# Optimization experiments

Measured on AMD Instinct MI355X. Metric: run time of the kernel, lower is better.

Reference implementation:

```python
import jax, jax.numpy as jnp
import numpy as np

REPEAT = 75  # upsample_repeat
UP = 4       # upsample_convs[0]


def setup_inputs() -> dict:
    key = jax.random.key(0)
    ks = jax.random.split(key, 12)
    B, L, F = 4, 48, 80
    C, H, A = 256, 896, 256  # conditional_size, rnn_size, signal_channels
    T = L * UP * REPEAT
    def xav(k, shape, fan_in):
        return jax.random.normal(k, shape, jnp.float32) * (1.0 / np.sqrt(fan_in))
    return {
        "local_features": jax.random.normal(ks[0], (B, L, F), jnp.float32),
        "gold_signal": jax.random.uniform(ks[1], (B, T), jnp.float32, -1.0, 1.0),
        "proj_w": xav(ks[2], (C, F), F),
        "proj_b": jnp.zeros((C,), jnp.float32),
        "up_w": xav(ks[3], (C, C, UP), C),
        "up_b": jnp.zeros((C,), jnp.float32),
        "embed_w": xav(ks[4], (C,), 1),
        "embed_b": jnp.zeros((C,), jnp.float32),
        "gru_wi": xav(ks[5], (3 * H, C), C),
        "gru_wh": xav(ks[6], (3 * H, H), H),
        "gru_bi": jnp.zeros((3 * H,), jnp.float32),
        "gru_bh": jnp.zeros((3 * H,), jnp.float32),
        "out_w1": xav(ks[7], (H, H), H),
        "out_b1": jnp.zeros((H,), jnp.float32),
        "out_w2": xav(ks[8], (A, H), H),
        "out_b2": jnp.zeros((A,), jnp.float32),
    }


def _forward(local_features, gold_signal, proj_w, proj_b, up_w, up_b,
             embed_w, embed_b, gru_wi, gru_wh, gru_bi, gru_bh,
             out_w1, out_b1, out_w2, out_b2):
    B = local_features.shape[0]
    O = up_w.shape[0]
    # --- conditional feature upsample ---
    # 1x1 conv: [B,L,F] -> [B,C,L]
    x = jnp.einsum("blf,cf->bcl", local_features, proj_w) + proj_b[None, :, None]
    # transposed conv, kernel=stride=UP: [B,C,L] -> [B,C,L*UP]
    x = jnp.einsum("bcl,ock->bolk", x, up_w).reshape(B, O, -1) + up_b[None, :, None]
    cond = jnp.repeat(x, REPEAT, axis=2)  # [B,C,T]
    # --- embed gold signal (1x1 conv, in_channels=1) ---
    sig = gold_signal[:, None, :] * embed_w[None, :, None] + embed_b[None, :, None]
    feats = (sig + cond).transpose(2, 0, 1)  # [T,B,C]
    # --- GRU (torch semantics), precompute input projections ---
    xp = feats @ gru_wi.T + gru_bi  # [T,B,3H]
    H = gru_wh.shape[1]

    def step(h, xpt):
        gh = h @ gru_wh.T + gru_bh
        xr, xz, xn = jnp.split(xpt, 3, axis=-1)
        hr, hz, hn = jnp.split(gh, 3, axis=-1)
        r = jax.nn.sigmoid(xr + hr)
        z = jax.nn.sigmoid(xz + hz)
        n = jnp.tanh(xn + r * hn)
        h_new = (1.0 - z) * n + z * h
        return h_new, h_new

    h0 = jnp.zeros((B, H), feats.dtype)
    _, hs = jax.lax.scan(step, h0, xp)  # [T,B,H]
    # --- output MLP + log-softmax over channels ---
    y = jax.nn.relu(hs @ out_w1.T + out_b1)
    logits = y @ out_w2.T + out_b2  # [T,B,A]
    logp = jax.nn.log_softmax(logits, axis=2)
    return logp.transpose(1, 2, 0)  # [B,A,T]


def reference(local_features, gold_signal, proj_w, proj_b, up_w, up_b,
              embed_w, embed_b, gru_wi, gru_wh, gru_bi, gru_bh,
              out_w1, out_b1, out_w2, out_b2):
    return _forward(local_features, gold_signal, proj_w, proj_b, up_w, up_b,
                    embed_w, embed_b, gru_wi, gru_wh, gru_bi, gru_bh,
                    out_w1, out_b1, out_w2, out_b2)
```

## Files before the change

### kernel.cpp

```cpp
#include <hip/hip_runtime.h>
#include <hip/hip_bf16.h>

#define B_ 4
#define L_ 48
#define F_ 80
#define C_ 256
#define H_ 896
#define G3_ 2688
#define A_ 256
#define T_ 14400
#define NBLK_ 192
#define REP_ 75

#define NMEM 28
#define RPW 12
#define NREAL 112
#define GRU_GRID 256
#define DYN_LDS 81920

typedef _Float16 __attribute__((ext_vector_type(8))) f16x8;
typedef __attribute__((ext_vector_type(4))) float f32x4;
typedef _Float16 __attribute__((ext_vector_type(2))) half2_;

__device__ __forceinline__ float fdot2f16(unsigned int a, unsigned int b, float c){
  return __builtin_amdgcn_fdot2(__builtin_bit_cast(half2_, a), __builtin_bit_cast(half2_, b), c, false);
}
__device__ __forceinline__ unsigned short f2h(float x){
  return __builtin_bit_cast(unsigned short, (_Float16)x);
}
__device__ __forceinline__ unsigned int packh2(float a, float b){
  return (unsigned int)f2h(a) | ((unsigned int)f2h(b) << 16);
}

template<int CTRL>
__device__ __forceinline__ float dppadd(float x){
  int r = __builtin_amdgcn_update_dpp(0, __builtin_bit_cast(int, x), CTRL, 0xF, 0xF, true);
  return x + __builtin_bit_cast(float, r);
}
__device__ __forceinline__ float wred(float x){
  x = dppadd<0xB1>(x);
  x = dppadd<0x4E>(x);
  x = dppadd<0x124>(x);
  x = dppadd<0x128>(x);
  x = dppadd<0x142>(x);
  x = dppadd<0x143>(x);
  return x;
}

__device__ __forceinline__ void ld7_llc(const unsigned int* base, unsigned int* hd){
  asm volatile(
    "global_load_dword %0, %7, off sc0 sc1\n\t"
    "global_load_dword %1, %7, off offset:256 sc0 sc1\n\t"
    "global_load_dword %2, %7, off offset:512 sc0 sc1\n\t"
    "global_load_dword %3, %7, off offset:768 sc0 sc1\n\t"
    "global_load_dword %4, %7, off offset:1024 sc0 sc1\n\t"
    "global_load_dword %5, %7, off offset:1280 sc0 sc1\n\t"
    "global_load_dword %6, %7, off offset:1536 sc0 sc1\n\t"
    "s_waitcnt vmcnt(0)"
    : "=&v"(hd[0]), "=&v"(hd[1]), "=&v"(hd[2]), "=&v"(hd[3]),
      "=&v"(hd[4]), "=&v"(hd[5]), "=&v"(hd[6])
    : "v"(base)
    : "memory");
}

__global__ void k_transpose_pw(const float* __restrict__ pw, float* __restrict__ pwT){
  int idx = blockIdx.x * 256 + threadIdx.x;
  if (idx >= F_ * C_) return;
  int f = idx / C_, c = idx % C_;
  pwT[idx] = pw[c * F_ + f];
}

__global__ void k_x1(const float* __restrict__ lf, const float* __restrict__ pwT,
                     const float* __restrict__ pb, float* __restrict__ x1){
  int bl = blockIdx.x;
  int c = threadIdx.x;
  const float* lrow = lf + (size_t)bl * F_;
  float acc = pb[c];
  for (int f = 0; f < F_; ++f) acc = fmaf(lrow[f], pwT[f * C_ + c], acc);
  x1[(size_t)bl * C_ + c] = acc;
}

__global__ void k_transpose_up(const float* __restrict__ up, float* __restrict__ upT){
  int idx = blockIdx.x * 256 + threadIdx.x;
  int o = idx % C_, c = (idx / C_) % C_, k = idx / (C_ * C_);
  upT[idx] = up[(o * C_ + c) * 4 + k];
}

__global__ void k_cond(const float* __restrict__ upT, const float* __restrict__ x1,
                       const float* __restrict__ ub, float* __restrict__ cond){
  int bblk = blockIdx.x;
  int blk = bblk % NBLK_;
  int b = bblk / NBLK_;
  int l = blk >> 2, kk = blk & 3;
  int o = threadIdx.x;
  const float* x1row = x1 + ((size_t)b * L_ + l) * C_;
  const float* uT = upT + (size_t)kk * C_ * C_;
  float acc = ub[o];
  for (int c = 0; c < C_; ++c) acc = fmaf(x1row[c], uT[c * C_ + o], acc);
  cond[(size_t)bblk * C_ + o] = acc;
}

__global__ void k_transpose_wi(const float* __restrict__ wi, float* __restrict__ wiT){
  int idx = blockIdx.x * 256 + threadIdx.x;
  int g = idx % G3_, c = idx / G3_;
  wiT[idx] = wi[(size_t)g * C_ + c];
}

__global__ void k_v(const float* __restrict__ wiT, const float* __restrict__ eb,
                    const float* __restrict__ cond, const float* __restrict__ bi,
                    float* __restrict__ v){
  int idx = blockIdx.x * 512 + threadIdx.x;
  int g = idx % G3_;
  int bblk = idx / G3_;
  const float* crow = cond + (size_t)bblk * C_;
  float acc = bi[g];
  for (int c = 0; c < C_; ++c) acc = fmaf(eb[c] + crow[c], wiT[(size_t)c * G3_ + g], acc);
  v[idx] = acc;
}

__global__ void k_u(const float* __restrict__ wiT, const float* __restrict__ ew,
                    float* __restrict__ u){
  int g = blockIdx.x * 256 + threadIdx.x;
  if (g >= G3_) return;
  float acc = 0.f;
  for (int c = 0; c < C_; ++c) acc = fmaf(ew[c], wiT[(size_t)c * G3_ + g], acc);
  u[g] = acc;
}

__global__ void k_packwh(const float* __restrict__ wh, unsigned int* __restrict__ whp){
  int idx = blockIdx.x * 256 + threadIdx.x;
  int lane = idx & 63;
  int r2 = idx >> 6;
  int dw = r2 % 7; int r3 = r2 / 7;
  int i = r3 % RPW; int W = r3 / RPW;
  int g = (i >> 2) * H_ + W * 4 + (i & 3);
  int k = dw * 128 + lane * 2;
  const float* p = wh + (size_t)g * H_ + k;
  whp[idx] = packh2(p[0], p[1]);
}

__global__ void k_cvth(const float* __restrict__ src, unsigned short* __restrict__ dst, int n){
  int idx = blockIdx.x * 256 + threadIdx.x;
  if (idx >= n) return;
  dst[idx] = f2h(src[idx]);
}

__global__ __launch_bounds__(576, 1) void k_gru(
    const float* __restrict__ gold, const float* __restrict__ v,
    const float* __restrict__ u, const float* __restrict__ bh,
    const unsigned int* __restrict__ whp,
    unsigned short* hsx)
{
  extern __shared__ unsigned int dynls[];
  const int bid = blockIdx.x;
  const int tid = threadIdx.x;
  const int wave = tid >> 6;
  const int lane = tid & 63;

  if (bid >= NREAL){
    volatile unsigned int* bflag = dynls;
    if (tid == 0) dynls[0] = 0;
    __syncthreads();
    const unsigned int* slotT = (const unsigned int*)(hsx + ((size_t)T_ * B_) * H_);
    float x = 1.0f + (float)tid * 1e-6f;
    float a = 1.0000001f, b = 0.9999999f;
    for (;;){
#pragma unroll 64
      for (int i = 0; i < 4096; ++i)
        asm volatile("v_fmac_f32 %0, %1, %2" : "+v"(x) : "v"(a), "v"(b));
      if (wave == 0){
        unsigned int d = ~0u;
        if (lane < 4){
          const unsigned int* pp = slotT + lane * 448;
          asm volatile("global_load_dword %0, %1, off sc0 sc1\n\ts_waitcnt vmcnt(0)"
                       : "=v"(d) : "v"(pp) : "memory");
        }
        bool ok = (lane < 4) ? (d != ~0u) : true;
        if (__all(ok) && lane == 0) *bflag = 1u;
      }
      if (*bflag) break;
    }
    return;
  }

  const int batch = (bid & 7) >> 1;
  const int m = ((bid >> 3) << 1) | (bid & 1);
  unsigned int (*lds_h)[448] = (unsigned int(*)[448])dynls;

  if (wave == 8){
    for (int t = 0; t < T_; ++t){
      const unsigned int* hp =
          (const unsigned int*)(hsx + ((size_t)t * B_ + batch) * H_) + lane;
      unsigned int hd[7];
      for (;;){
        ld7_llc(hp, hd);
        bool ok = (hd[0] != ~0u) & (hd[1] != ~0u) & (hd[2] != ~0u) &
                  (hd[3] != ~0u) & (hd[4] != ~0u) & (hd[5] != ~0u) & (hd[6] != ~0u);
        if (__all(ok)) break;
      }
#pragma unroll
      for (int dw = 0; dw < 7; ++dw) lds_h[t & 1][dw * 64 + lane] = hd[dw];
      __syncthreads();
    }
    return;
  }

  const int W = m * 8 + wave;

  unsigned int wreg[RPW][7];
#pragma unroll
  for (int i = 0; i < RPW; ++i){
    const unsigned int* p = whp + ((size_t)(W * RPW + i) * 7) * 64 + lane;
#pragma unroll
    for (int dw = 0; dw < 7; ++dw) wreg[i][dw] = p[dw * 64];
  }

  const bool owner = (lane >= 48) && (lane < 52);
  const int jj = lane - 48;
  const int jg = 4 * W + (jj & 3);
  float u3[3] = {0,0,0}, bh3[3] = {0,0,0}, v3[3] = {0,0,0}, v3n[3] = {0,0,0};
  float hcur = 0.f;
  if (owner){
    u3[0] = u[jg]; u3[1] = u[jg + H_]; u3[2] = u[jg + 2 * H_];
    bh3[0] = bh[jg]; bh3[1] = bh[jg + H_]; bh3[2] = bh[jg + 2 * H_];
    const float* vp = v + ((size_t)(batch * NBLK_)) * G3_ + jg;
    v3[0] = vp[0]; v3[1] = vp[H_]; v3[2] = vp[2 * H_];
  }
  const float* goldb = gold + (size_t)batch * T_;
  int cnt = 0, blkc = 0;

  for (int t = 0; t < T_; ++t){
    float go = goldb[t];
    __syncthreads();
    unsigned int hd[7];
#pragma unroll
    for (int dw = 0; dw < 7; ++dw) hd[dw] = lds_h[t & 1][dw * 64 + lane];

    float acc[RPW];
#pragma unroll
    for (int i = 0; i < RPW; ++i){
      float a = 0.f;
#pragma unroll
      for (int dw = 0; dw < 7; ++dw) a = fdot2f16(wreg[i][dw], hd[dw], a);
      acc[i] = wred(a);
    }

    if (owner){
      if (cnt == REP_ - 2){
        int nb = blkc + 1; if (nb > NBLK_ - 1) nb = NBLK_ - 1;
        const float* vp = v + ((size_t)(batch * NBLK_ + nb)) * G3_ + jg;
        v3n[0] = vp[0]; v3n[1] = vp[H_]; v3n[2] = vp[2 * H_];
      }
      float hr = jj==0 ? acc[0] : jj==1 ? acc[1] : jj==2 ? acc[2]  : acc[3];
      float hz = jj==0 ? acc[4] : jj==1 ? acc[5] : jj==2 ? acc[6]  : acc[7];
      float hn = jj==0 ? acc[8] : jj==1 ? acc[9] : jj==2 ? acc[10] : acc[11];
      hr += bh3[0]; hz += bh3[1]; hn += bh3[2];
      float xr = fmaf(go, u3[0], v3[0]);
      float xz = fmaf(go, u3[1], v3[1]);
      float xn = fmaf(go, u3[2], v3[2]);
      float r = 1.f / (1.f + __expf(-(xr + hr)));
      float z = 1.f / (1.f + __expf(-(xz + hz)));
      float e = __expf(2.f * (xn + r * hn));
      float n = 1.f - 2.f / (e + 1.f);
      float hnew = (1.f - z) * n + z * hcur;
      hcur = hnew;
      unsigned int h16 = (unsigned int)f2h(hnew);
      unsigned int oth = (unsigned int)__builtin_amdgcn_update_dpp(
          0, (int)h16, 0xB1, 0xF, 0xF, true);
      unsigned int packed = h16 | (oth << 16);
      unsigned int p23 = (unsigned int)__builtin_amdgcn_update_dpp(
          0, (int)packed, 0x4E, 0xF, 0xF, true);
      if (jj == 0){
        unsigned long long v64 = (unsigned long long)packed
                               | ((unsigned long long)p23 << 32);
        unsigned long long* dst =
            (unsigned long long*)((unsigned int*)(hsx + ((size_t)(t + 1) * B_ + batch) * H_)
                                  + 2 * W);
        __hip_atomic_store(dst, v64, __ATOMIC_RELAXED, __HIP_MEMORY_SCOPE_AGENT);
      }
    }
    if (++cnt == REP_){
      cnt = 0; ++blkc;
      v3[0] = v3n[0]; v3[1] = v3n[1]; v3[2] = v3n[2];
    }
  }
}

__global__ __launch_bounds__(256) void k_mlp(
    const unsigned short* hs, const unsigned short* __restrict__ w1h,
    const unsigned short* __restrict__ w2h, const float* __restrict__ ob1,
    const float* __restrict__ ob2, float* logits)
{
  const int mtile = blockIdx.x * 32;
  const int tid = threadIdx.x;
  const int wid = tid >> 6, lane = tid & 63;
  const int l15 = lane & 15, l4 = lane >> 4;
  __shared__ unsigned short y_lds[32 * 904];

  for (int nblk = 0; nblk < 14; ++nblk){
    f32x4 acc[2] = {(f32x4)(0.f), (f32x4)(0.f)};
    const int colg = nblk * 64 + wid * 16 + l15;
    for (int kk = 0; kk < 28; ++kk){
      const int k = kk * 32 + l4 * 8;
      f16x8 bfrag = *(const f16x8*)(w1h + (size_t)colg * H_ + k);
#pragma unroll
      for (int mf = 0; mf < 2; ++mf){
        f16x8 afrag = *(const f16x8*)(hs + (size_t)(mtile + mf * 16 + l15) * H_ + k);
        acc[mf] = __builtin_amdgcn_mfma_f32_16x16x32_f16(afrag, bfrag, acc[mf], 0, 0, 0);
      }
    }
    float bias = ob1[colg];
#pragma unroll
    for (int mf = 0; mf < 2; ++mf)
#pragma unroll
      for (int rg = 0; rg < 4; ++rg){
        float yv = acc[mf][rg] + bias;
        yv = yv > 0.f ? yv : 0.f;
        y_lds[(mf * 16 + l4 * 4 + rg) * 904 + colg] = f2h(yv);
      }
  }
  __syncthreads();

  f32x4 a2acc[2][4];
#pragma unroll
  for (int mf = 0; mf < 2; ++mf)
#pragma unroll
    for (int nf = 0; nf < 4; ++nf) a2acc[mf][nf] = (f32x4)(0.f);

  for (int kk = 0; kk < 28; ++kk){
    const int k = kk * 32 + l4 * 8;
    f16x8 a2[2];
#pragma unroll
    for (int mf = 0; mf < 2; ++mf)
      a2[mf] = *(const f16x8*)(&y_lds[(mf * 16 + l15) * 904 + k]);
#pragma unroll
    for (int nf = 0; nf < 4; ++nf){
      const int col = wid * 64 + nf * 16 + l15;
      f16x8 bfrag = *(const f16x8*)(w2h + (size_t)col * H_ + k);
#pragma unroll
      for (int mf = 0; mf < 2; ++mf)
        a2acc[mf][nf] = __builtin_amdgcn_mfma_f32_16x16x32_f16(a2[mf], bfrag, a2acc[mf][nf], 0, 0, 0);
    }
  }
#pragma unroll
  for (int nf = 0; nf < 4; ++nf){
    const int col = wid * 64 + nf * 16 + l15;
    const float bias = ob2[col];
#pragma unroll
    for (int mf = 0; mf < 2; ++mf)
#pragma unroll
      for (int rg = 0; rg < 4; ++rg){
        const int mrow = mtile + mf * 16 + l4 * 4 + rg;
        logits[(size_t)mrow * 448 + col] = a2acc[mf][nf][rg] + bias;
      }
  }
}

__global__ __launch_bounds__(256) void k_softmax(const float* __restrict__ logits,
                                                 float* __restrict__ out)
{
  const int bid = blockIdx.x;
  const int b = bid / 225;
  const int t0 = (bid % 225) * 64;
  const int tid = threadIdx.x;
  __shared__ float pm[64][4];
  __shared__ float ps[64][4];
  __shared__ float lz[64];
  {
    const int r = tid >> 2, q = tid & 3;
    const float* row = logits + (size_t)((t0 + r) * 4 + b) * 448 + q * 64;
    float mx = -1e30f;
    for (int j = 0; j < 64; ++j) mx = fmaxf(mx, row[j]);
    float s = 0.f;
    for (int j = 0; j < 64; ++j) s += __expf(row[j] - mx);
    pm[r][q] = mx; ps[r][q] = s;
  }
  __syncthreads();
  if (tid < 64){
    float m0 = pm[tid][0], m1 = pm[tid][1], m2 = pm[tid][2], m3 = pm[tid][3];
    float mx = fmaxf(fmaxf(m0, m1), fmaxf(m2, m3));
    float s = ps[tid][0] * __expf(m0 - mx) + ps[tid][1] * __expf(m1 - mx)
            + ps[tid][2] * __expf(m2 - mx) + ps[tid][3] * __expf(m3 - mx);
    lz[tid] = mx + logf(s);
  }
  __syncthreads();
  for (int i = 0; i < 64; ++i){
    const int idx = i * 256 + tid;
    const int a = idx >> 6, tt = idx & 63;
    float x = logits[(size_t)((t0 + tt) * 4 + b) * 448 + a];
    out[((size_t)(b * A_) + a) * T_ + t0 + tt] = x - lz[tt];
  }
}

extern "C" void kernel_launch(void* const* d_in, const int* in_sizes, int n_in,
                              void* d_out, int out_size, void* d_ws, size_t ws_size,
                              hipStream_t stream)
{
  (void)in_sizes; (void)n_in; (void)out_size; (void)ws_size;
  const float* lf   = (const float*)d_in[0];
  const float* gold = (const float*)d_in[1];
  const float* pw   = (const float*)d_in[2];
  const float* pb   = (const float*)d_in[3];
  const float* upw  = (const float*)d_in[4];
  const float* upb  = (const float*)d_in[5];
  const float* ew   = (const float*)d_in[6];
  const float* eb   = (const float*)d_in[7];
  const float* wi   = (const float*)d_in[8];
  const float* wh   = (const float*)d_in[9];
  const float* bi   = (const float*)d_in[10];
  const float* bhp  = (const float*)d_in[11];
  const float* w1   = (const float*)d_in[12];
  const float* b1   = (const float*)d_in[13];
  const float* w2   = (const float*)d_in[14];
  const float* b2   = (const float*)d_in[15];
  float* out = (float*)d_out;
  char* ws = (char*)d_ws;

  size_t off = 0;
  auto take = [&](size_t bytes){
    size_t r = off; off += (bytes + 255) & ~(size_t)255; return r;
  };
  float* pwT  = (float*)(ws + take((size_t)F_ * C_ * 4));
  float* x1   = (float*)(ws + take((size_t)B_ * L_ * C_ * 4));
  float* upT  = (float*)(ws + take((size_t)4 * C_ * C_ * 4));
  float* cond = (float*)(ws + take((size_t)B_ * NBLK_ * C_ * 4));
  float* wiT  = (float*)(ws + take((size_t)C_ * G3_ * 4));
  float* v    = (float*)(ws + take((size_t)B_ * NBLK_ * G3_ * 4));
  float* u    = (float*)(ws + take((size_t)G3_ * 4));
  unsigned int*   whp = (unsigned int*)(ws + take((size_t)224 * RPW * 7 * 64 * 4));
  unsigned short* w1h = (unsigned short*)(ws + take((size_t)H_ * H_ * 2));
  unsigned short* w2h = (unsigned short*)(ws + take((size_t)A_ * H_ * 2));
  unsigned short* hsx = (unsigned short*)(ws + take((size_t)(T_ + 1) * B_ * H_ * 2));

  hipFuncSetAttribute((const void*)k_gru,
                      hipFuncAttributeMaxDynamicSharedMemorySize, DYN_LDS);

  hipMemsetAsync((void*)hsx, 0, (size_t)B_ * H_ * 2, stream);
  hipMemsetAsync((void*)(hsx + (size_t)B_ * H_), 0xFF, (size_t)T_ * B_ * H_ * 2, stream);

  k_transpose_pw<<<80, 256, 0, stream>>>(pw, pwT);
  k_x1<<<B_ * L_, 256, 0, stream>>>(lf, pwT, pb, x1);
  k_transpose_up<<<1024, 256, 0, stream>>>(upw, upT);
  k_cond<<<B_ * NBLK_, 256, 0, stream>>>(upT, x1, upb, cond);
  k_transpose_wi<<<2688, 256, 0, stream>>>(wi, wiT);
  k_v<<<4032, 512, 0, stream>>>(wiT, eb, cond, bi, v);
  k_u<<<11, 256, 0, stream>>>(wiT, ew, u);
  k_packwh<<<4704, 256, 0, stream>>>(wh, whp);
  k_cvth<<<(H_ * H_ + 255) / 256, 256, 0, stream>>>(w1, w1h, H_ * H_);
  k_cvth<<<(A_ * H_ + 255) / 256, 256, 0, stream>>>(w2, w2h, A_ * H_);

  k_gru<<<GRU_GRID, 576, DYN_LDS, stream>>>(gold, v, u, bhp, whp, hsx);

  const unsigned short* hs_mlp = hsx + (size_t)B_ * H_;
  float* logits = (float*)hsx + (size_t)B_ * 448;
  k_mlp<<<1800, 256, 0, stream>>>(hs_mlp, w1h, w2h, b1, b2, logits);
  k_softmax<<<900, 256, 0, stream>>>(logits, out);
}
```

Baseline: 37.48 ms.

## Fuse output MLP into GRU kernel as concurrent consumer blocks

The spare blocks of the persistent GRU launch used to spin on dummy FMAs. They now run the output MLP tile by tile, each tile starting once the hidden states it needs have been published (polled with a sleep backoff). This overlaps the MLP with the serial recurrence and removes the separate MLP launch. The LDS-feeding wave also issues coherent prefetch loads a few steps ahead to warm the cache. The risks are that logits are written in place over hidden-state rows while the GRU is still running, and that the extra memory traffic and lost heater blocks may slow the latency-critical recurrence.

```diff
diff --git a/kernel.cpp b/kernel.cpp
--- a/kernel.cpp
+++ b/kernel.cpp
@@ -15,8 +15,8 @@
 #define NMEM 28
 #define RPW 12
 #define NREAL 112
-#define GRU_GRID 256
-#define DYN_LDS 81920
+#define NMLP 128
+#define NTILE 1800
 
 typedef _Float16 __attribute__((ext_vector_type(8))) f16x8;
 typedef __attribute__((ext_vector_type(4))) float f32x4;
@@ -148,44 +148,107 @@
 __global__ __launch_bounds__(576, 1) void k_gru(
     const float* __restrict__ gold, const float* __restrict__ v,
     const float* __restrict__ u, const float* __restrict__ bh,
-    const unsigned int* __restrict__ whp,
-    unsigned short* hsx)
+    const unsigned int* __restrict__ whp, unsigned short* hsx,
+    const unsigned short* __restrict__ w1h, const unsigned short* __restrict__ w2h,
+    const float* __restrict__ ob1, const float* __restrict__ ob2,
+    float* logits)
 {
-  extern __shared__ unsigned int dynls[];
+  __shared__ __attribute__((aligned(16))) unsigned char smem[32 * 904 * 2];
   const int bid = blockIdx.x;
   const int tid = threadIdx.x;
   const int wave = tid >> 6;
   const int lane = tid & 63;
 
   if (bid >= NREAL){
-    volatile unsigned int* bflag = dynls;
-    if (tid == 0) dynls[0] = 0;
-    __syncthreads();
-    const unsigned int* slotT = (const unsigned int*)(hsx + ((size_t)T_ * B_) * H_);
-    float x = 1.0f + (float)tid * 1e-6f;
-    float a = 1.0000001f, b = 0.9999999f;
-    for (;;){
-#pragma unroll 64
-      for (int i = 0; i < 4096; ++i)
-        asm volatile("v_fmac_f32 %0, %1, %2" : "+v"(x) : "v"(a), "v"(b));
+    unsigned short* y_lds = (unsigned short*)smem;
+    const unsigned short* hs = hsx + (size_t)B_ * H_;
+    const int wid = tid >> 6;
+    const int l15 = lane & 15, l4 = lane >> 4;
+    for (int k2 = bid - NREAL; k2 < NTILE; k2 += NMLP){
       if (wave == 0){
-        unsigned int d = ~0u;
-        if (lane < 4){
-          const unsigned int* pp = slotT + lane * 448;
-          asm volatile("global_load_dword %0, %1, off sc0 sc1\n\ts_waitcnt vmcnt(0)"
-                       : "=v"(d) : "v"(pp) : "memory");
+        const unsigned int* sp0 =
+            (const unsigned int*)(hsx + ((size_t)(8 * k2 + 8) * B_) * H_);
+        for (;;){
+          unsigned int hd[7]; bool ok = true;
+#pragma unroll
+          for (int b = 0; b < B_; ++b){
+            ld7_llc(sp0 + (size_t)b * 448 + lane, hd);
+            ok &= (hd[0]!=~0u)&(hd[1]!=~0u)&(hd[2]!=~0u)&(hd[3]!=~0u)
+                 &(hd[4]!=~0u)&(hd[5]!=~0u)&(hd[6]!=~0u);
+          }
+          if (__all(ok)) break;
+          __builtin_amdgcn_s_sleep(127);
         }
-        bool ok = (lane < 4) ? (d != ~0u) : true;
-        if (__all(ok) && lane == 0) *bflag = 1u;
-      }
-      if (*bflag) break;
+      }
+      __syncthreads();
+      const int mtile = k2 * 32;
+      if (tid < 256){
+        for (int nblk = 0; nblk < 14; ++nblk){
+          f32x4 acc[2] = {(f32x4)(0.f), (f32x4)(0.f)};
+          const int colg = nblk * 64 + wid * 16 + l15;
+          for (int kk = 0; kk < 28; ++kk){
+            const int k = kk * 32 + l4 * 8;
+            f16x8 bfrag = *(const f16x8*)(w1h + (size_t)colg * H_ + k);
+#pragma unroll
+            for (int mf = 0; mf < 2; ++mf){
+              f16x8 afrag = *(const f16x8*)(hs + (size_t)(mtile + mf * 16 + l15) * H_ + k);
+              acc[mf] = __builtin_amdgcn_mfma_f32_16x16x32_f16(afrag, bfrag, acc[mf], 0, 0, 0);
+            }
+          }
+          float bias = ob1[colg];
+#pragma unroll
+          for (int mf = 0; mf < 2; ++mf)
+#pragma unroll
+            for (int rg = 0; rg < 4; ++rg){
+              float yv = acc[mf][rg] + bias;
+              yv = yv > 0.f ? yv : 0.f;
+              y_lds[(mf * 16 + l4 * 4 + rg) * 904 + colg] = f2h(yv);
+            }
+        }
+      }
+      __syncthreads();
+      if (tid < 256){
+        f32x4 a2acc[2][4];
+#pragma unroll
+        for (int mf = 0; mf < 2; ++mf)
+#pragma unroll
+          for (int nf = 0; nf < 4; ++nf) a2acc[mf][nf] = (f32x4)(0.f);
+        for (int kk = 0; kk < 28; ++kk){
+          const int k = kk * 32 + l4 * 8;
+          f16x8 a2[2];
+#pragma unroll
+          for (int mf = 0; mf < 2; ++mf)
+            a2[mf] = *(const f16x8*)(&y_lds[(mf * 16 + l15) * 904 + k]);
+#pragma unroll
+          for (int nf = 0; nf < 4; ++nf){
+            const int col = wid * 64 + nf * 16 + l15;
+            f16x8 bfrag = *(const f16x8*)(w2h + (size_t)col * H_ + k);
+#pragma unroll
+            for (int mf = 0; mf < 2; ++mf)
+              a2acc[mf][nf] = __builtin_amdgcn_mfma_f32_16x16x32_f16(a2[mf], bfrag, a2acc[mf][nf], 0, 0, 0);
+          }
+        }
+#pragma unroll
+        for (int nf = 0; nf < 4; ++nf){
+          const int col = wid * 64 + nf * 16 + l15;
+          const float bias = ob2[col];
+#pragma unroll
+          for (int mf = 0; mf < 2; ++mf)
+#pragma unroll
+            for (int rg = 0; rg < 4; ++rg){
+              const int mrow = mtile + mf * 16 + l4 * 4 + rg;
+              logits[(size_t)mrow * 448 + col] = a2acc[mf][nf][rg] + bias;
+            }
+        }
+      }
+      __syncthreads();
     }
     return;
   }
 
   const int batch = (bid & 7) >> 1;
   const int m = ((bid >> 3) << 1) | (bid & 1);
-  unsigned int (*lds_h)[448] = (unsigned int(*)[448])dynls;
+  unsigned int (*lds_h)[448] = (unsigned int(*)[448])smem;
 
   if (wave == 8){
     for (int t = 0; t < T_; ++t){
@@ -200,6 +263,17 @@
       }
 #pragma unroll
       for (int dw = 0; dw < 7; ++dw) lds_h[t & 1][dw * 64 + lane] = hd[dw];
+      {
+        int tw = t + 4; if (tw > T_) tw = T_;
+        const unsigned int* wp =
+            (const unsigned int*)(hsx + ((size_t)tw * B_ + batch) * H_) + lane;
+#pragma unroll
+        for (int dw = 0; dw < 7; ++dw){
+          unsigned int dummy;
+          asm volatile("global_load_dword %0, %1, off sc0 sc1"
+                       : "=v"(dummy) : "v"(wp + dw * 64) : "memory");
+        }
+      }
       __syncthreads();
     }
     return;
@@ -286,76 +360,6 @@
   }
 }
 
-__global__ __launch_bounds__(256) void k_mlp(
-    const unsigned short* hs, const unsigned short* __restrict__ w1h,
-    const unsigned short* __restrict__ w2h, const float* __restrict__ ob1,
-    const float* __restrict__ ob2, float* logits)
-{
-  const int mtile = blockIdx.x * 32;
-  const int tid = threadIdx.x;
-  const int wid = tid >> 6, lane = tid & 63;
-  const int l15 = lane & 15, l4 = lane >> 4;
-  __shared__ unsigned short y_lds[32 * 904];
-
-  for (int nblk = 0; nblk < 14; ++nblk){
-    f32x4 acc[2] = {(f32x4)(0.f), (f32x4)(0.f)};
-    const int colg = nblk * 64 + wid * 16 + l15;
-    for (int kk = 0; kk < 28; ++kk){
-      const int k = kk * 32 + l4 * 8;
-      f16x8 bfrag = *(const f16x8*)(w1h + (size_t)colg * H_ + k);
-#pragma unroll
-      for (int mf = 0; mf < 2; ++mf){
-        f16x8 afrag = *(const f16x8*)(hs + (size_t)(mtile + mf * 16 + l15) * H_ + k);
-        acc[mf] = __builtin_amdgcn_mfma_f32_16x16x32_f16(afrag, bfrag, acc[mf], 0, 0, 0);
-      }
-    }
-    float bias = ob1[colg];
-#pragma unroll
-    for (int mf = 0; mf < 2; ++mf)
-#pragma unroll
-      for (int rg = 0; rg < 4; ++rg){
-        float yv = acc[mf][rg] + bias;
-        yv = yv > 0.f ? yv : 0.f;
-        y_lds[(mf * 16 + l4 * 4 + rg) * 904 + colg] = f2h(yv);
-      }
-  }
-  __syncthreads();
-
-  f32x4 a2acc[2][4];
-#pragma unroll
-  for (int mf = 0; mf < 2; ++mf)
-#pragma unroll
-    for (int nf = 0; nf < 4; ++nf) a2acc[mf][nf] = (f32x4)(0.f);
-
-  for (int kk = 0; kk < 28; ++kk){
-    const int k = kk * 32 + l4 * 8;
-    f16x8 a2[2];
-#pragma unroll
-    for (int mf = 0; mf < 2; ++mf)
-      a2[mf] = *(const f16x8*)(&y_lds[(mf * 16 + l15) * 904 + k]);
-#pragma unroll
-    for (int nf = 0; nf < 4; ++nf){
-      const int col = wid * 64 + nf * 16 + l15;
-      f16x8 bfrag = *(const f16x8*)(w2h + (size_t)col * H_ + k);
-#pragma unroll
-      for (int mf = 0; mf < 2; ++mf)
-        a2acc[mf][nf] = __builtin_amdgcn_mfma_f32_16x16x32_f16(a2[mf], bfrag, a2acc[mf][nf], 0, 0, 0);
-    }
-  }
-#pragma unroll
-  for (int nf = 0; nf < 4; ++nf){
-    const int col = wid * 64 + nf * 16 + l15;
-    const float bias = ob2[col];
-#pragma unroll
-    for (int mf = 0; mf < 2; ++mf)
-#pragma unroll
-      for (int rg = 0; rg < 4; ++rg){
-        const int mrow = mtile + mf * 16 + l4 * 4 + rg;
-        logits[(size_t)mrow * 448 + col] = a2acc[mf][nf][rg] + bias;
-      }
-  }
-}
-
 __global__ __launch_bounds__(256) void k_softmax(const float* __restrict__ logits,
                                                  float* __restrict__ out)
 {
@@ -432,9 +436,6 @@
   unsigned short* w2h = (unsigned short*)(ws + take((size_t)A_ * H_ * 2));
   unsigned short* hsx = (unsigned short*)(ws + take((size_t)(T_ + 1) * B_ * H_ * 2));
 
-  hipFuncSetAttribute((const void*)k_gru,
-                      hipFuncAttributeMaxDynamicSharedMemorySize, DYN_LDS);
-
   hipMemsetAsync((void*)hsx, 0, (size_t)B_ * H_ * 2, stream);
   hipMemsetAsync((void*)(hsx + (size_t)B_ * H_), 0xFF, (size_t)T_ * B_ * H_ * 2, stream);
 
@@ -449,10 +450,8 @@
   k_cvth<<<(H_ * H_ + 255) / 256, 256, 0, stream>>>(w1, w1h, H_ * H_);
   k_cvth<<<(A_ * H_ + 255) / 256, 256, 0, stream>>>(w2, w2h, A_ * H_);
 
-  k_gru<<<GRU_GRID, 576, DYN_LDS, stream>>>(gold, v, u, bhp, whp, hsx);
-
-  const unsigned short* hs_mlp = hsx + (size_t)B_ * H_;
   float* logits = (float*)hsx + (size_t)B_ * 448;
-  k_mlp<<<1800, 256, 0, stream>>>(hs_mlp, w1h, w2h, b1, b2, logits);
+  k_gru<<<NREAL + NMLP, 576, 0, stream>>>(gold, v, u, bhp, whp, hsx,
+                                          w1h, w2h, b1, b2, logits);
   k_softmax<<<900, 256, 0, stream>>>(logits, out);
 }
```

Result: slower. 38.55 ms (+2.8%).
